# Kernel optimization log

Hardware: AMD Instinct MI355X
Metric: run time of the kernel (lower is better)

Reference implementation:

```python
import jax, jax.numpy as jnp
import numpy as np

B, T, F, U = 32, 128, 128, 128  # batch, seq_length, feature dim, lstm units


def setup_inputs() -> dict:
    key = jax.random.key(0)
    ks = jax.random.split(key, 5)
    X = jax.random.normal(ks[0], (B, T, F), dtype=jnp.float32)
    # Dense(seq_length) over concat([X, s_repeated]) -> weight [(F+U), T]
    Wd = jax.random.normal(ks[1], (F + U, T), dtype=jnp.float32) / np.sqrt(F + U)
    bd = jnp.zeros((T,), jnp.float32)
    # Keras LSTM params, gate order i,f,c,o packed along last axis
    Wk = jax.random.normal(ks[2], (F, 4 * U), dtype=jnp.float32) / np.sqrt(F)
    Wr = jax.random.normal(ks[3], (U, 4 * U), dtype=jnp.float32) / np.sqrt(U)
    bl = jnp.zeros((4 * U,), jnp.float32)
    return {"X": X, "Wd": Wd, "bd": bd, "Wk": Wk, "Wr": Wr, "bl": bl}


def reference(X, Wd, bd, Wk, Wr, bl):
    Bq, Tq, Fq = X.shape
    Uq = Wr.shape[0]

    def step(s, i):
        # s: attention query carried across steps (= previous h_state)
        s_rep = jnp.broadcast_to(s[:, None, :], (Bq, Tq, Uq))
        concat_X = jnp.concatenate([X, s_rep], axis=-1)           # [B,T,F+U]
        alphas = jax.nn.softmax(concat_X @ Wd + bd, axis=1)        # [B,T,T], softmax over seq axis
        alpha_i = alphas[:, :, i]                                  # [B,T] (only column i is used)
        ctx = jnp.einsum('bt,btf->bf', alpha_i, X)                 # [B,F] weighted sum
        # Keras LSTM called with initial_state=None each step -> h0 = c0 = 0
        h0 = jnp.zeros((Bq, Uq), X.dtype)
        c0 = jnp.zeros((Bq, Uq), X.dtype)
        z = ctx @ Wk + h0 @ Wr + bl                                # [B,4U]
        zi, zf, zc, zo = jnp.split(z, 4, axis=-1)
        c = jax.nn.sigmoid(zf) * c0 + jax.nn.sigmoid(zi) * jnp.tanh(zc)
        h = jax.nn.sigmoid(zo) * jnp.tanh(c)                       # [B,U]
        return h, h  # new query s = h_state; per-step output = lstm_out[:, 0, :]

    s0 = jnp.zeros((Bq, Uq), X.dtype)
    _, outs = jax.lax.scan(step, s0, jnp.arange(Tq))               # [T,B,U]
    return jnp.transpose(outs, (1, 0, 2))                          # [B,T,U]
```

## Files before the change

### kernel.cpp

```cpp
#include <hip/hip_runtime.h>

namespace {

constexpr int Bq = 32;
constexpr int Tq = 128;
constexpr int Fq = 128;
constexpr int Uq = 128;
constexpr int PITCH  = 129;
constexpr int APITCH = 20;
constexpr int CPITCH = 132;
constexpr int ITILE  = 16;

__device__ __forceinline__ float sigmoid_(float x) {
  return 1.0f / (1.0f + __expf(-x));
}
__device__ __forceinline__ float tanh_(float x) {
  x = fminf(20.0f, fmaxf(-20.0f, x));
  const float e = __expf(2.0f * x);
  return (e - 1.0f) / (e + 1.0f);
}

__global__ __launch_bounds__(512) void k_all(const float* __restrict__ X,
                                             const float* __restrict__ Wd,
                                             const float* __restrict__ Wk,
                                             const float* __restrict__ bl,
                                             float* __restrict__ out) {
  __shared__ float Xs[Tq * PITCH];
  __shared__ float SB[Tq * APITCH > ITILE * CPITCH ?
                      Tq * APITCH : ITILE * CPITCH];
  float* As = SB;
  float* Cs = SB;
  const int tid = threadIdx.x;
  const int b = blockIdx.y;
  const int i0b = blockIdx.x * ITILE;

  const float* Xb = X + b * (Tq * Fq);
#pragma unroll
  for (int it = 0; it < 8; ++it) {
    const int e = tid + it * 512;
    const int t = e >> 5;
    const int f4 = e & 31;
    const float4 v = reinterpret_cast<const float4*>(Xb)[e];
    float* d = &Xs[t * PITCH + f4 * 4];
    d[0] = v.x; d[1] = v.y; d[2] = v.z; d[3] = v.w;
  }
  __syncthreads();

  const int lane = tid & 63;
  const int wv = tid >> 6;
  const int iL = wv * 2;
  const int i0 = __builtin_amdgcn_readfirstlane(i0b + iL);

  float a0[2] = {0.f, 0.f}, a1[2] = {0.f, 0.f};
  const float* Wp = Wd + i0;
  const float* xr0 = &Xs[lane * PITCH];
  const float* xr1 = &Xs[(lane + 64) * PITCH];
#pragma unroll 8
  for (int f = 0; f < Fq; ++f) {
    const float x0 = xr0[f];
    const float x1 = xr1[f];
    const float* wr = Wp + f * Tq;
#pragma unroll
    for (int j = 0; j < 2; ++j) {
      const float w = wr[j];
      a0[j] = fmaf(x0, w, a0[j]);
      a1[j] = fmaf(x1, w, a1[j]);
    }
  }

  float p0[2], p1[2];
#pragma unroll
  for (int j = 0; j < 2; ++j) {
    float m = fmaxf(a0[j], a1[j]);
#pragma unroll
    for (int d = 1; d < 64; d <<= 1) m = fmaxf(m, __shfl_xor(m, d, 64));
    const float e0 = __expf(a0[j] - m);
    const float e1 = __expf(a1[j] - m);
    float s = e0 + e1;
#pragma unroll
    for (int d = 1; d < 64; d <<= 1) s += __shfl_xor(s, d, 64);
    const float inv = 1.0f / s;
    p0[j] = e0 * inv;
    p1[j] = e1 * inv;
  }

  *reinterpret_cast<float2*>(&As[lane * APITCH + iL]) = make_float2(p0[0], p0[1]);
  *reinterpret_cast<float2*>(&As[(lane + 64) * APITCH + iL]) =
      make_float2(p1[0], p1[1]);
  __syncthreads();

  float c0[2] = {0.f, 0.f}, c1[2] = {0.f, 0.f};
#pragma unroll 8
  for (int t = 0; t < Tq; ++t) {
    const float2 a2 = *reinterpret_cast<const float2*>(&As[t * APITCH + iL]);
    const float aa[2] = {a2.x, a2.y};
    const float x0 = Xs[t * PITCH + lane];
    const float x1 = Xs[t * PITCH + lane + 64];
#pragma unroll
    for (int j = 0; j < 2; ++j) {
      c0[j] = fmaf(aa[j], x0, c0[j]);
      c1[j] = fmaf(aa[j], x1, c1[j]);
    }
  }
  __syncthreads();
#pragma unroll
  for (int j = 0; j < 2; ++j) {
    Cs[(iL + j) * CPITCH + lane] = c0[j];
    Cs[(iL + j) * CPITCH + lane + 64] = c1[j];
  }
  __syncthreads();

  const int uu = lane & 31;
  const int ub = (wv & 3) * 32 + uu;
  const int ig = ((wv >> 2) << 1) | (lane >> 5);
  const int ih = ig * 4;
  float zi[4] = {0.f, 0.f, 0.f, 0.f};
  float zc[4] = {0.f, 0.f, 0.f, 0.f};
  float zo[4] = {0.f, 0.f, 0.f, 0.f};

  const float* WkP = Wk + ub;
  for (int f = 0; f < Fq; f += 4) {
    float4 cr[4];
#pragma unroll
    for (int j = 0; j < 4; ++j)
      cr[j] = *reinterpret_cast<const float4*>(&Cs[(ih + j) * CPITCH + f]);
#pragma unroll
    for (int ff = 0; ff < 4; ++ff) {
      const float* wf = WkP + (f + ff) * (4 * Uq);
      const float wi = wf[0];
      const float wc = wf[2 * Uq];
      const float wo = wf[3 * Uq];
#pragma unroll
      for (int j = 0; j < 4; ++j) {
        const float cv = (&cr[j].x)[ff];
        zi[j] = fmaf(cv, wi, zi[j]);
        zc[j] = fmaf(cv, wc, zc[j]);
        zo[j] = fmaf(cv, wo, zo[j]);
      }
    }
  }

  const float bi = bl[ub];
  const float bc = bl[2 * Uq + ub];
  const float bo = bl[3 * Uq + ub];
#pragma unroll
  for (int j = 0; j < 4; ++j) {
    const float cc = sigmoid_(zi[j] + bi) * tanh_(zc[j] + bc);
    const float h = sigmoid_(zo[j] + bo) * tanh_(cc);
    out[(b * Tq + i0b + ih + j) * Uq + ub] = h;
  }
}

}

extern "C" void kernel_launch(void* const* d_in, const int* in_sizes, int n_in,
                              void* d_out, int out_size, void* d_ws, size_t ws_size,
                              hipStream_t stream) {
  const float* X  = (const float*)d_in[0];
  const float* Wd = (const float*)d_in[1];
  const float* Wk = (const float*)d_in[3];
  const float* bl = (const float*)d_in[5];
  float* out = (float*)d_out;

  k_all<<<dim3(8, 32), 512, 0, stream>>>(X, Wd, Wk, bl, out);
}
```

Before: 88.09 us.

## Split softmax across two wave groups and keep transposed X tile in LDS

```diff
diff --git a/kernel.cpp b/kernel.cpp
--- a/kernel.cpp
+++ b/kernel.cpp
@@ -6,10 +6,8 @@
 constexpr int Tq = 128;
 constexpr int Fq = 128;
 constexpr int Uq = 128;
-constexpr int PITCH  = 129;
-constexpr int APITCH = 20;
-constexpr int CPITCH = 132;
-constexpr int ITILE  = 16;
+constexpr int PITCH = 132;
+constexpr int ITILE = 16;
 
 __device__ __forceinline__ float sigmoid_(float x) {
   return 1.0f / (1.0f + __expf(-x));
@@ -26,94 +24,133 @@
                                              const float* __restrict__ bl,
                                              float* __restrict__ out) {
   __shared__ float Xs[Tq * PITCH];
-  __shared__ float SB[Tq * APITCH > ITILE * CPITCH ?
-                      Tq * APITCH : ITILE * CPITCH];
-  float* As = SB;
-  float* Cs = SB;
+  __shared__ float Xt[Fq * PITCH];
+  __shared__ float Cs[ITILE * PITCH];
+  __shared__ float SmM[2][ITILE];
+  __shared__ float SmS[2][ITILE];
   const int tid = threadIdx.x;
   const int b = blockIdx.y;
   const int i0b = blockIdx.x * ITILE;
-
   const float* Xb = X + b * (Tq * Fq);
+
 #pragma unroll
   for (int it = 0; it < 8; ++it) {
     const int e = tid + it * 512;
     const int t = e >> 5;
     const int f4 = e & 31;
     const float4 v = reinterpret_cast<const float4*>(Xb)[e];
-    float* d = &Xs[t * PITCH + f4 * 4];
-    d[0] = v.x; d[1] = v.y; d[2] = v.z; d[3] = v.w;
+    *reinterpret_cast<float4*>(&Xs[t * PITCH + f4 * 4]) = v;
+  }
+#pragma unroll
+  for (int it = 0; it < 8; ++it) {
+    const int e = tid + it * 512;
+    const int f = e & 127;
+    const int t4 = e >> 7;
+    float4 v;
+    v.x = Xb[(t4 * 4 + 0) * Fq + f];
+    v.y = Xb[(t4 * 4 + 1) * Fq + f];
+    v.z = Xb[(t4 * 4 + 2) * Fq + f];
+    v.w = Xb[(t4 * 4 + 3) * Fq + f];
+    *reinterpret_cast<float4*>(&Xt[f * PITCH + t4 * 4]) = v;
   }
   __syncthreads();
 
   const int lane = tid & 63;
   const int wv = tid >> 6;
-  const int iL = wv * 2;
+  const int tg = wv >> 2;
+  const int ig = wv & 3;
+  const int iL = ig * 4;
   const int i0 = __builtin_amdgcn_readfirstlane(i0b + iL);
-
-  float a0[2] = {0.f, 0.f}, a1[2] = {0.f, 0.f};
+  const int t = tg * 64 + lane;
+
+  float a[4] = {0.f, 0.f, 0.f, 0.f};
+  const float* xr = &Xs[t * PITCH];
   const float* Wp = Wd + i0;
-  const float* xr0 = &Xs[lane * PITCH];
-  const float* xr1 = &Xs[(lane + 64) * PITCH];
-#pragma unroll 8
-  for (int f = 0; f < Fq; ++f) {
-    const float x0 = xr0[f];
-    const float x1 = xr1[f];
-    const float* wr = Wp + f * Tq;
-#pragma unroll
-    for (int j = 0; j < 2; ++j) {
-      const float w = wr[j];
-      a0[j] = fmaf(x0, w, a0[j]);
-      a1[j] = fmaf(x1, w, a1[j]);
-    }
-  }
-
-  float p0[2], p1[2];
-#pragma unroll
-  for (int j = 0; j < 2; ++j) {
-    float m = fmaxf(a0[j], a1[j]);
-#pragma unroll
-    for (int d = 1; d < 64; d <<= 1) m = fmaxf(m, __shfl_xor(m, d, 64));
-    const float e0 = __expf(a0[j] - m);
-    const float e1 = __expf(a1[j] - m);
-    float s = e0 + e1;
-#pragma unroll
-    for (int d = 1; d < 64; d <<= 1) s += __shfl_xor(s, d, 64);
-    const float inv = 1.0f / s;
-    p0[j] = e0 * inv;
-    p1[j] = e1 * inv;
-  }
-
-  *reinterpret_cast<float2*>(&As[lane * APITCH + iL]) = make_float2(p0[0], p0[1]);
-  *reinterpret_cast<float2*>(&As[(lane + 64) * APITCH + iL]) =
-      make_float2(p1[0], p1[1]);
-  __syncthreads();
-
-  float c0[2] = {0.f, 0.f}, c1[2] = {0.f, 0.f};
-#pragma unroll 8
-  for (int t = 0; t < Tq; ++t) {
-    const float2 a2 = *reinterpret_cast<const float2*>(&As[t * APITCH + iL]);
-    const float aa[2] = {a2.x, a2.y};
-    const float x0 = Xs[t * PITCH + lane];
-    const float x1 = Xs[t * PITCH + lane + 64];
-#pragma unroll
-    for (int j = 0; j < 2; ++j) {
-      c0[j] = fmaf(aa[j], x0, c0[j]);
-      c1[j] = fmaf(aa[j], x1, c1[j]);
-    }
-  }
-  __syncthreads();
-#pragma unroll
-  for (int j = 0; j < 2; ++j) {
-    Cs[(iL + j) * CPITCH + lane] = c0[j];
-    Cs[(iL + j) * CPITCH + lane + 64] = c1[j];
+#pragma unroll 4
+  for (int f4 = 0; f4 < 32; ++f4) {
+    const float4 x = *reinterpret_cast<const float4*>(&xr[f4 * 4]);
+#pragma unroll
+    for (int k = 0; k < 4; ++k) {
+      const float* wr = Wp + (f4 * 4 + k) * Tq;
+      const float xv = (&x.x)[k];
+#pragma unroll
+      for (int j = 0; j < 4; ++j) a[j] = fmaf(xv, wr[j], a[j]);
+    }
+  }
+
+  float m[4], e[4], s[4];
+#pragma unroll
+  for (int j = 0; j < 4; ++j) {
+    float mw = a[j];
+#pragma unroll
+    for (int d = 1; d < 64; d <<= 1) mw = fmaxf(mw, __shfl_xor(mw, d, 64));
+    const float ee = __expf(a[j] - mw);
+    float ss = ee;
+#pragma unroll
+    for (int d = 1; d < 64; d <<= 1) ss += __shfl_xor(ss, d, 64);
+    m[j] = mw; e[j] = ee; s[j] = ss;
+  }
+  if (lane == 0) {
+#pragma unroll
+    for (int j = 0; j < 4; ++j) {
+      SmM[tg][iL + j] = m[j];
+      SmS[tg][iL + j] = s[j];
+    }
+  }
+  __syncthreads();
+  float p[4];
+#pragma unroll
+  for (int j = 0; j < 4; ++j) {
+    const float mo = SmM[tg ^ 1][iL + j];
+    const float so = SmS[tg ^ 1][iL + j];
+    const float gm = fmaxf(m[j], mo);
+    const float sc = __expf(m[j] - gm);
+    const float S = s[j] * sc + so * __expf(mo - gm);
+    p[j] = e[j] * (sc / S);
+  }
+
+  float c0[4] = {0.f, 0.f, 0.f, 0.f};
+  float c1[4] = {0.f, 0.f, 0.f, 0.f};
+  const int tb = tg * 64;
+  const float* xtr0 = &Xt[lane * PITCH + tb];
+  const float* xtr1 = &Xt[(lane + 64) * PITCH + tb];
+#pragma unroll 4
+  for (int q = 0; q < 16; ++q) {
+    const float4 x0 = *reinterpret_cast<const float4*>(&xtr0[q * 4]);
+    const float4 x1 = *reinterpret_cast<const float4*>(&xtr1[q * 4]);
+#pragma unroll
+    for (int k = 0; k < 4; ++k) {
+      const float xa = (&x0.x)[k];
+      const float xb = (&x1.x)[k];
+#pragma unroll
+      for (int j = 0; j < 4; ++j) {
+        const float aj = __shfl(p[j], q * 4 + k, 64);
+        c0[j] = fmaf(aj, xa, c0[j]);
+        c1[j] = fmaf(aj, xb, c1[j]);
+      }
+    }
+  }
+  if (tg == 0) {
+#pragma unroll
+    for (int j = 0; j < 4; ++j) {
+      Cs[(iL + j) * PITCH + lane] = c0[j];
+      Cs[(iL + j) * PITCH + lane + 64] = c1[j];
+    }
+  }
+  __syncthreads();
+  if (tg == 1) {
+#pragma unroll
+    for (int j = 0; j < 4; ++j) {
+      Cs[(iL + j) * PITCH + lane] += c0[j];
+      Cs[(iL + j) * PITCH + lane + 64] += c1[j];
+    }
   }
   __syncthreads();
 
   const int uu = lane & 31;
   const int ub = (wv & 3) * 32 + uu;
-  const int ig = ((wv >> 2) << 1) | (lane >> 5);
-  const int ih = ig * 4;
+  const int ig3 = ((wv >> 2) << 1) | (lane >> 5);
+  const int ih = ig3 * 4;
   float zi[4] = {0.f, 0.f, 0.f, 0.f};
   float zc[4] = {0.f, 0.f, 0.f, 0.f};
   float zo[4] = {0.f, 0.f, 0.f, 0.f};
@@ -123,7 +160,7 @@
     float4 cr[4];
 #pragma unroll
     for (int j = 0; j < 4; ++j)
-      cr[j] = *reinterpret_cast<const float4*>(&Cs[(ih + j) * CPITCH + f]);
+      cr[j] = *reinterpret_cast<const float4*>(&Cs[(ih + j) * PITCH + f]);
 #pragma unroll
     for (int ff = 0; ff < 4; ++ff) {
       const float* wf = WkP + (f + ff) * (4 * Uq);
```

After: 88.79 us. Within noise of the previous version (+0.8%).
